# Kernel optimization log

Hardware: AMD Instinct MI355X
Metric: run time of the kernel (lower is better)

The kernel has to match this reference:

```python
import jax, jax.numpy as jnp
import numpy as np

B, N, D = 4, 1024, 1024
H = 16
RS, RC = 32, 32
MLP = int(D * 4.0)
EPS = 1e-6


def _ln(x):
    # LayerNorm with no scale/bias (flax defaults: eps=1e-6)
    m = jnp.mean(x, axis=-1, keepdims=True)
    v = jnp.mean(jnp.square(x - m), axis=-1, keepdims=True)
    return (x - m) * jax.lax.rsqrt(v + EPS)


def _rms(x, scale):
    rms = jnp.sqrt(jnp.mean(jnp.square(x), axis=-1, keepdims=True) + EPS)
    return scale * x / rms


def _modulate(x, shift, scale):
    return x * (1 + scale[:, None]) + shift[:, None]


def setup_inputs() -> dict:
    key = jax.random.key(0)
    ks = jax.random.split(key, 20)
    s = 0.02
    return {
        'x': jax.random.normal(ks[0], (B, N, D), jnp.float32),
        'c': jax.random.normal(ks[1], (B, D), jnp.float32),
        'cls_token': jax.random.normal(ks[2], (B, D), jnp.float32),
        'Wc': jax.random.normal(ks[3], (D, 6 * D), jnp.float32) * s,
        'bc': jax.random.normal(ks[4], (6 * D,), jnp.float32) * s,
        'Wqkv': jax.random.normal(ks[5], (D, 3 * D), jnp.float32) * s,
        'bqkv': jnp.zeros((3 * D,), jnp.float32),
        'Wo': jax.random.normal(ks[6], (D, D), jnp.float32) * s,
        'bo': jnp.zeros((D,), jnp.float32),
        'A_s': jax.random.normal(ks[7], (D, RS), jnp.float32) * s,
        'B_s': jax.random.normal(ks[8], (RS, D), jnp.float32) * s,
        'rms_s_scale': jnp.ones((D,), jnp.float32),
        'C_r': jax.random.normal(ks[9], (D, RC), jnp.float32) * s,
        'D_r': jax.random.normal(ks[10], (RC, D), jnp.float32) * s,
        'rms_c_scale': jnp.ones((D,), jnp.float32),
        'W1': jax.random.normal(ks[11], (D, MLP), jnp.float32) * s,
        'b1': jnp.zeros((MLP,), jnp.float32),
        'W2': jax.random.normal(ks[12], (MLP, D), jnp.float32) * s,
        'b2': jnp.zeros((D,), jnp.float32),
    }


def reference(x, c, cls_token, Wc, bc, Wqkv, bqkv, Wo, bo, A_s, B_s,
              rms_s_scale, C_r, D_r, rms_c_scale, W1, b1, W2, b2):
    hd = D // H
    # AdaLN conditioning
    c_proj = jax.nn.silu(c) @ Wc + bc                    # (B, 6D)
    shift_a, scale_a, gate_a, shift_m, scale_m, gate_m = jnp.split(c_proj, 6, axis=-1)

    # Self-attention branch
    x_norm = _modulate(_ln(x), shift_a, scale_a)         # (B, N, D)
    qkv = x_norm @ Wqkv + bqkv                           # (B, N, 3D)
    q, k, v = jnp.split(qkv, 3, axis=-1)
    q = q.reshape(B, N, H, hd).transpose(0, 2, 1, 3)     # (B, H, N, hd)
    k = k.reshape(B, N, H, hd).transpose(0, 2, 1, 3)
    v = v.reshape(B, N, H, hd).transpose(0, 2, 1, 3)
    attn_w = jax.nn.softmax(jnp.einsum('bhqd,bhkd->bhqk', q, k) * hd ** (-0.5), axis=-1)
    attn_out = jnp.einsum('bhqk,bhkd->bhqd', attn_w, v)
    attn_out = attn_out.transpose(0, 2, 1, 3).reshape(B, N, D)
    attn_out = attn_out @ Wo + bo
    Y = x + gate_a[:, None] * attn_out

    # Self-gram low-rank branch (residual)
    gram_s = (x @ A_s) @ B_s                             # (B, N, D)
    X_prime = _rms(gram_s, rms_s_scale) + Y

    # Cross-gram branch via CLS token (no residual)
    u_c = cls_token[:, :, None] * C_r[None]              # (B, D, RC)
    v_c = jnp.einsum('bnd,bdr->bnr', X_prime, u_c)       # (B, N, RC)
    gram_c = v_c @ D_r                                   # (B, N, D)
    Z = _rms(gram_c, rms_c_scale)

    # MLP branch
    z_norm = _modulate(_ln(Z), shift_m, scale_m)
    h = jax.nn.gelu(z_norm @ W1 + b1) @ W2 + b2
    return Z + gate_m[:, None] * h
```

## Files before the change

kernel.cpp:

```cpp
#include <hip/hip_runtime.h>
#include <stdint.h>

typedef float  f32x4  __attribute__((ext_vector_type(4)));
typedef short  s16x8  __attribute__((ext_vector_type(8)));
typedef __bf16 bf16x4 __attribute__((ext_vector_type(4)));
typedef __bf16 bf16x8 __attribute__((ext_vector_type(8)));

#define D_    1024
#define SIXD  6144
#define QSCALE 0.18033688011112042f

#define BAR() asm volatile("s_barrier" ::: "memory")

__device__ __forceinline__ f32x4 mfma_b(const s16x8 &a, const s16x8 &b, const f32x4 &c) {
  return __builtin_amdgcn_mfma_f32_16x16x32_bf16(a, b, c, 0, 0, 0);
}

__device__ __forceinline__ void gload_lds16(const void* g, void* l) {
  __builtin_amdgcn_global_load_lds(
      (const __attribute__((address_space(1))) uint32_t*)g,
      (__attribute__((address_space(3))) uint32_t*)l, 16, 0, 0);
}

__global__ __launch_bounds__(256)
void prep(const float* __restrict__ c, const float* __restrict__ Wc,
          const float* __restrict__ bc, float* __restrict__ cproj,
          const float* __restrict__ Wqkv, const float* __restrict__ Wo,
          const float* __restrict__ W1, const float* __restrict__ W2,
          __bf16* __restrict__ Wqkvt, __bf16* __restrict__ Wot,
          __bf16* __restrict__ W1t, __bf16* __restrict__ W2t)
{
  __shared__ __align__(16) char smem[33280];
  int tid = threadIdx.x;
  if (blockIdx.x < 192) {
    float* sc = (float*)smem;
    float (*tp)[4][32] = (float(*)[4][32])(smem + 16384);
    for (int i = tid; i < 4096; i += 256) {
      float v = c[i];
      sc[i] = v / (1.f + __expf(-v));
    }
    __syncthreads();
    int colo = tid & 31, kseg = tid >> 5;
    int col = blockIdx.x * 32 + colo;
    float a0 = 0.f, a1 = 0.f, a2 = 0.f, a3 = 0.f;
    for (int k = kseg * 128; k < kseg * 128 + 128; k++) {
      float w = Wc[(size_t)k * SIXD + col];
      a0 += sc[k] * w; a1 += sc[1024 + k] * w;
      a2 += sc[2048 + k] * w; a3 += sc[3072 + k] * w;
    }
    tp[kseg][0][colo] = a0; tp[kseg][1][colo] = a1;
    tp[kseg][2][colo] = a2; tp[kseg][3][colo] = a3;
    __syncthreads();
    if (kseg == 0) {
#pragma unroll
      for (int b = 0; b < 4; b++) {
        float s = bc[col];
#pragma unroll
        for (int g = 0; g < 8; g++) s += tp[g][b][colo];
        cproj[b * SIXD + col] = s;
      }
    }
    return;
  }
  int bid = blockIdx.x - 192;
  const float* W; __bf16* Wt; int Kdim, Ndim, lb;
  if (bid < 192)      { W = Wqkv; Wt = Wqkvt; Kdim = 1024; Ndim = 3072; lb = bid; }
  else if (bid < 256) { W = Wo;   Wt = Wot;   Kdim = 1024; Ndim = 1024; lb = bid - 192; }
  else if (bid < 512) { W = W1;   Wt = W1t;   Kdim = 1024; Ndim = 4096; lb = bid - 256; }
  else                { W = W2;   Wt = W2t;   Kdim = 4096; Ndim = 1024; lb = bid - 512; }
  int ntn = Ndim >> 6;
  int ktg = lb / ntn, nt = lb % ntn;
  __bf16* tt = (__bf16*)smem;
  const float* src = W + (size_t)(ktg * 256) * Ndim + nt * 64;
  int krow = tid >> 4, c4 = tid & 15;
#pragma unroll
  for (int t = 0; t < 4; t++) {
#pragma unroll
    for (int i = 0; i < 4; i++) {
      int k = i * 16 + krow;
      float4 v = ((const float4*)(src + (size_t)(t * 64 + k) * Ndim))[c4];
      __bf16* row = tt + (t * 64 + k) * 65 + c4 * 4;
      row[0] = (__bf16)v.x; row[1] = (__bf16)v.y;
      row[2] = (__bf16)v.z; row[3] = (__bf16)v.w;
    }
  }
  __syncthreads();
  __bf16* dst = Wt + (size_t)(nt * 64) * Kdim + ktg * 256;
  int n = tid >> 2, ks = (tid & 3) * 16;
#pragma unroll
  for (int t = 0; t < 4; t++) {
    bf16x8 lo, hi;
#pragma unroll
    for (int j = 0; j < 8; j++) {
      lo[j] = tt[(t * 64 + ks + j) * 65 + n];
      hi[j] = tt[(t * 64 + ks + 8 + j) * 65 + n];
    }
    __bf16* dp = dst + (size_t)n * Kdim + t * 64 + ks;
    *(bf16x8*)(dp) = lo;
    *(bf16x8*)(dp + 8) = hi;
  }
}

__global__ __launch_bounds__(256)
void ln_mod(const float* __restrict__ X, const float* __restrict__ cproj,
            int shift_off, int scale_off, __bf16* __restrict__ Out)
{
  int row = blockIdx.x;
  int b = row >> 10;
  int tid = threadIdx.x;
  const float4* xr = (const float4*)(X + (size_t)row * D_);
  float4 v = xr[tid];
  float s  = v.x + v.y + v.z + v.w;
  float s2 = v.x * v.x + v.y * v.y + v.z * v.z + v.w * v.w;
#pragma unroll
  for (int off = 1; off < 64; off <<= 1) {
    s  += __shfl_xor(s,  off, 64);
    s2 += __shfl_xor(s2, off, 64);
  }
  __shared__ float red[8];
  int wave = tid >> 6, lane = tid & 63;
  if (lane == 0) { red[wave] = s; red[4 + wave] = s2; }
  __syncthreads();
  s  = red[0] + red[1] + red[2] + red[3];
  s2 = red[4] + red[5] + red[6] + red[7];
  float mean = s * (1.f / D_);
  float var  = s2 * (1.f / D_) - mean * mean;
  float rstd = rsqrtf(var + 1e-6f);
  const float4* sh = (const float4*)(cproj + b * SIXD + shift_off);
  const float4* sc = (const float4*)(cproj + b * SIXD + scale_off);
  float4 shv = sh[tid], scv = sc[tid];
  bf16x4 o;
  o[0] = (__bf16)((v.x - mean) * rstd * (1.f + scv.x) + shv.x);
  o[1] = (__bf16)((v.y - mean) * rstd * (1.f + scv.y) + shv.y);
  o[2] = (__bf16)((v.z - mean) * rstd * (1.f + scv.z) + shv.z);
  o[3] = (__bf16)((v.w - mean) * rstd * (1.f + scv.w) + shv.w);
  *(bf16x4*)(Out + (size_t)row * D_ + tid * 4) = o;
}

template<int EPI, int NBUF>
__global__ __launch_bounds__(256)
void gemm_bt(const __bf16* __restrict__ A, const __bf16* __restrict__ Bt,
             const float* __restrict__ bias, const float* __restrict__ cproj,
             int gate_off, const float* __restrict__ resid,
             void* __restrict__ Cout, void* __restrict__ Cout2,
             void* __restrict__ Cout3, void* __restrict__ Cout4,
             int M, int N, int K, int SK)
{
  __shared__ __align__(16) __bf16 As[NBUF * 128 * 32];
  __shared__ __align__(16) __bf16 Bs[NBUF * 128 * 32];
  const int PD = NBUF - 1;
  int tilesN = N >> 7, tilesM = M >> 7;
  int npersk = tilesM * tilesN;
  int sk = blockIdx.x / npersk;
  int rest = blockIdx.x % npersk;
  int cpx = npersk >> 3;
  rest = (rest & 7) * cpx + (rest >> 3);
  int bm = rest / tilesN, bn = rest % tilesN;
  int Klen = K / SK, Kstart = sk * Klen;

  int tid = threadIdx.x;
  int lane = tid & 63, wave = tid >> 6;
  int lr = lane & 15, lg = lane >> 4;
  int wm = (wave >> 1) << 6, wn = (wave & 1) << 6;

  f32x4 acc[4][4] = {};

  int sr = tid >> 2, skb = tid & 3;
  int scol = ((skb ^ ((sr >> 1) & 3)) * 8);
  const __bf16* pa = A + (size_t)((bm << 7) + sr) * K + Kstart + scol;
  const __bf16* pb = Bt + (size_t)((bn << 7) + sr) * K + Kstart + scol;
  const size_t rstep = (size_t)64 * K;
  __bf16* la = As + tid * 8;
  __bf16* lb = Bs + tid * 8;

  auto STAGE = [&](int buf, int k0) {
    int bo = buf * 4096;
    gload_lds16(pa + k0, la + bo);
    gload_lds16(pa + rstep + k0, la + bo + 2048);
    gload_lds16(pb + k0, lb + bo);
    gload_lds16(pb + rstep + k0, lb + bo + 2048);
  };

  int nt = Klen >> 5;
#pragma unroll
  for (int p = 0; p < PD; p++) STAGE(p, p * 32);

  for (int t = 0; t < nt; t++) {
    if (t + PD < nt) STAGE((t + PD) % NBUF, (t + PD) * 32);
    int ahead = nt - 1 - t; if (ahead > PD) ahead = PD;
    if (ahead >= 3)      asm volatile("s_waitcnt vmcnt(12)" ::: "memory");
    else if (ahead == 2) asm volatile("s_waitcnt vmcnt(8)" ::: "memory");
    else if (ahead == 1) asm volatile("s_waitcnt vmcnt(4)" ::: "memory");
    else                 asm volatile("s_waitcnt vmcnt(0)" ::: "memory");
    BAR();
    const __bf16* Ac = As + (t % NBUF) * 4096;
    const __bf16* Bc = Bs + (t % NBUF) * 4096;
    s16x8 af[4], bfv[4];
#pragma unroll
    for (int m = 0; m < 4; m++) {
      int row = wm + m * 16 + lr;
      af[m] = *(const s16x8*)(Ac + row * 32 + ((lg ^ ((row >> 1) & 3)) * 8));
    }
#pragma unroll
    for (int n = 0; n < 4; n++) {
      int row = wn + n * 16 + lr;
      bfv[n] = *(const s16x8*)(Bc + row * 32 + ((lg ^ ((row >> 1) & 3)) * 8));
    }
    asm volatile("s_waitcnt lgkmcnt(0)" ::: "memory");
    __builtin_amdgcn_sched_barrier(0);
    BAR();
    __builtin_amdgcn_s_setprio(1);
#pragma unroll
    for (int m = 0; m < 4; m++)
#pragma unroll
      for (int n = 0; n < 4; n++)
        acc[m][n] = mfma_b(af[m], bfv[n], acc[m][n]);
    __builtin_amdgcn_s_setprio(0);
  }
  asm volatile("s_waitcnt vmcnt(0)" ::: "memory");

  int row0 = (bm << 7) + wm;
  int col0 = (bn << 7) + wn;
#pragma unroll
  for (int m = 0; m < 4; m++) {
#pragma unroll
    for (int n = 0; n < 4; n++) {
      int cc = col0 + n * 16 + lr;
      float bv = bias[cc];
#pragma unroll
      for (int r = 0; r < 4; r++) {
        int row = row0 + m * 16 + (lg << 2) + r;
        float v = acc[m][n][r] + bv;
        size_t idx = (size_t)row * N + cc;
        if (EPI == 0) {
          ((__bf16*)Cout)[idx] = (__bf16)v;
        } else if (EPI == 1) {
          int b = row >> 10;
          float g = cproj[b * SIXD + gate_off + cc];
          ((float*)Cout)[idx] = resid[idx] + g * v;
        }
      }
    }
  }
}

template<int EPI, int NT, int KD>
__global__ __launch_bounds__(512, 2)
void gemm256(const __bf16* __restrict__ A, const __bf16* __restrict__ Bt,
             const float* __restrict__ bias, const float* __restrict__ gcproj,
             void* __restrict__ Cout, void* __restrict__ Cout2,
             int M, int N)
{
  __shared__ __align__(16) __bf16 As[2 * 16384];
  __shared__ __align__(16) __bf16 Bs[2 * 16384];
  int tilesN = N >> 8, tilesM = M >> 8;
  int npersk = tilesM * tilesN;
  int sk = blockIdx.x / npersk;
  int rest = blockIdx.x % npersk;
  int cpx = npersk >> 3;
  rest = (rest & 7) * cpx + (rest >> 3);
  int bm = rest / tilesN, bn = rest % tilesN;
  int Kstart = sk * (NT * 64);

  int tid = threadIdx.x;
  int lane = tid & 63, wave = tid >> 6;
  int lr = lane & 15, lg = lane >> 4;
  int wr = wave >> 2, wc = wave & 3;

  f32x4 acc[8][4] = {};

  int srow = tid >> 3;
  int schunk = (tid & 7) ^ (srow & 7);
  const __bf16* pa = A  + (size_t)((bm << 8) + srow) * KD + Kstart + schunk * 8;
  const __bf16* pb = Bt + (size_t)((bn << 8) + srow) * KD + Kstart + schunk * 8;
  __bf16* la = As + tid * 8;
  __bf16* lb = Bs + tid * 8;

  auto SAq = [&](int t, int q) {
    gload_lds16(pa + (size_t)(q * 64) * KD + t * 64,
                la + (t & 1) * 16384 + q * 4096);
  };
  auto SBq = [&](int t, int q) {
    gload_lds16(pb + (size_t)(q * 64) * KD + t * 64,
                lb + (t & 1) * 16384 + q * 4096);
  };

#pragma unroll
  for (int q = 0; q < 4; q++) { SAq(0, q); }
#pragma unroll
  for (int q = 0; q < 4; q++) { SBq(0, q); }
#pragma unroll
  for (int q = 0; q < 4; q++) { SAq(1, q); }
#pragma unroll
  for (int q = 0; q < 4; q++) { SBq(1, q); }
  asm volatile("s_waitcnt vmcnt(8)" ::: "memory");
  BAR();

  int cc0 = ((lg ^ (lr & 7)) << 4);
  int cc1 = cc0 ^ 64;
  const char* aA = (const char*)As + (wr * 128 + lr) * 128;
  const char* aB = (const char*)Bs + (wc * 64 + lr) * 128;

  s16x8 alo[4][2], ahi[4][2], b0v[2][2], b1v[2][2];
#pragma unroll
  for (int m = 0; m < 4; m++) {
    alo[m][0] = *(const s16x8*)(aA + m * 2048 + cc0);
    alo[m][1] = *(const s16x8*)(aA + m * 2048 + cc1);
  }
#pragma unroll
  for (int n = 0; n < 2; n++) {
    b0v[n][0] = *(const s16x8*)(aB + n * 2048 + cc0);
    b0v[n][1] = *(const s16x8*)(aB + n * 2048 + cc1);
  }

  for (int t = 0; t < NT; t++) {
    const char* Ab = aA + (t & 1) * 32768;
    const char* Bb = aB + (t & 1) * 32768;

#pragma unroll
    for (int n = 0; n < 2; n++) {
      b1v[n][0] = *(const s16x8*)(Bb + 4096 + n * 2048 + cc0);
      b1v[n][1] = *(const s16x8*)(Bb + 4096 + n * 2048 + cc1);
    }
    __builtin_amdgcn_sched_barrier(0);
    __builtin_amdgcn_s_setprio(1);
#pragma unroll
    for (int m = 0; m < 4; m++)
#pragma unroll
      for (int n = 0; n < 2; n++) {
        acc[m][n] = mfma_b(alo[m][0], b0v[n][0], acc[m][n]);
        acc[m][n] = mfma_b(alo[m][1], b0v[n][1], acc[m][n]);
      }
    __builtin_amdgcn_s_setprio(0);
    asm volatile("s_waitcnt lgkmcnt(0)" ::: "memory");
    BAR();

#pragma unroll
    for (int m = 0; m < 4; m++) {
      ahi[m][0] = *(const s16x8*)(Ab + 8192 + m * 2048 + cc0);
      ahi[m][1] = *(const s16x8*)(Ab + 8192 + m * 2048 + cc1);
    }
    if (t + 2 < NT) { SBq(t + 2, 0); SBq(t + 2, 1); }
    __builtin_amdgcn_sched_barrier(0);
    __builtin_amdgcn_s_setprio(1);
#pragma unroll
    for (int m = 0; m < 4; m++)
#pragma unroll
      for (int n = 0; n < 2; n++) {
        acc[m][2 + n] = mfma_b(alo[m][0], b1v[n][0], acc[m][2 + n]);
        acc[m][2 + n] = mfma_b(alo[m][1], b1v[n][1], acc[m][2 + n]);
      }
    __builtin_amdgcn_s_setprio(0);
    asm volatile("s_waitcnt lgkmcnt(0)" ::: "memory");
    BAR();

    if (t + 2 < NT) {
      SBq(t + 2, 2); SBq(t + 2, 3);
      SAq(t + 2, 0); SAq(t + 2, 1); SAq(t + 2, 2); SAq(t + 2, 3);
    }
    __builtin_amdgcn_sched_barrier(0);
    __builtin_amdgcn_s_setprio(1);
#pragma unroll
    for (int m = 0; m < 4; m++)
#pragma unroll
      for (int n = 0; n < 2; n++) {
        acc[4 + m][2 + n] = mfma_b(ahi[m][0], b1v[n][0], acc[4 + m][2 + n]);
        acc[4 + m][2 + n] = mfma_b(ahi[m][1], b1v[n][1], acc[4 + m][2 + n]);
      }
#pragma unroll
    for (int m = 0; m < 4; m++)
#pragma unroll
      for (int n = 0; n < 2; n++) {
        acc[4 + m][n] = mfma_b(ahi[m][0], b0v[n][0], acc[4 + m][n]);
        acc[4 + m][n] = mfma_b(ahi[m][1], b0v[n][1], acc[4 + m][n]);
      }
    __builtin_amdgcn_s_setprio(0);
    if (t + 1 < NT) {
      if (t + 2 < NT) asm volatile("s_waitcnt vmcnt(8)" ::: "memory");
      else            asm volatile("s_waitcnt vmcnt(0)" ::: "memory");
      BAR();
      const char* An = aA + ((t + 1) & 1) * 32768;
      const char* Bn = aB + ((t + 1) & 1) * 32768;
#pragma unroll
      for (int m = 0; m < 4; m++) {
        alo[m][0] = *(const s16x8*)(An + m * 2048 + cc0);
        alo[m][1] = *(const s16x8*)(An + m * 2048 + cc1);
      }
#pragma unroll
      for (int n = 0; n < 2; n++) {
        b0v[n][0] = *(const s16x8*)(Bn + n * 2048 + cc0);
        b0v[n][1] = *(const s16x8*)(Bn + n * 2048 + cc1);
      }
    }
  }
  asm volatile("s_waitcnt lgkmcnt(0)" ::: "memory");

  int row0 = (bm << 8) + wr * 128;
  int col0 = (bn << 8) + wc * 64;
#pragma unroll
  for (int m = 0; m < 8; m++) {
#pragma unroll
    for (int n = 0; n < 4; n++) {
      int cc = col0 + n * 16 + lr;
      float bv;
      if (EPI == 6)      bv = (sk == 0) ? bias[cc] : 0.f;
      else               bv = bias[cc];
      if (EPI == 5 && cc >= 2048) {
        int rbase = row0 + m * 16 + (lg << 2);
        int dd = cc - 2048;
        int bb = rbase >> 10, ntok = rbase & 1023;
        bf16x4 o;
#pragma unroll
        for (int r = 0; r < 4; r++) o[r] = (__bf16)(acc[m][n][r] + bv);
        *(bf16x4*)((__bf16*)Cout2 + ((size_t)(bb << 10) + dd) * 1024 + ntok) = o;
        continue;
      }
#pragma unroll
      for (int r = 0; r < 4; r++) {
        int row = row0 + m * 16 + (lg << 2) + r;
        float v = acc[m][n][r] + bv;
        size_t idx = (size_t)row * N + cc;
        if (EPI == 2) {
          float u = 0.7978845608028654f * (v + 0.044715f * v * v * v);
          u = fminf(fmaxf(u, -15.f), 15.f);
          float e = __expf(2.f * u);
          float th = (e - 1.f) / (e + 1.f);
          ((__bf16*)Cout)[idx] = (__bf16)(0.5f * v * (1.f + th));
        } else if (EPI == 5) {
          float scq = (cc < 1024) ? QSCALE : 1.f;
          ((__bf16*)Cout)[idx] = (__bf16)(v * scq);
        } else if (EPI == 6) {
          int bb = row >> 10;
          float g = gcproj[bb * SIXD + 5120 + cc];
          atomicAdd((float*)Cout + idx, g * v);
        }
      }
    }
  }
}

__global__ __launch_bounds__(512, 4)
void attn_flash(const __bf16* __restrict__ qkv, const __bf16* __restrict__ Vt,
                __bf16* __restrict__ O)
{
  __shared__ __align__(16) __bf16 Kl[2][64 * 64];
  __shared__ __align__(16) __bf16 Vl[2][64 * 64];
  __shared__ __align__(16) __bf16 Pl[8][16 * 64];

  int bid = ((blockIdx.x & 7) << 6) | (blockIdx.x >> 3);
  int qt = bid & 7, h = (bid >> 3) & 15, b = bid >> 7;
  int tid = threadIdx.x, wave = tid >> 6, lane = tid & 63;
  int lr = lane & 15, lg = lane >> 4;

  size_t tok0 = (size_t)b * 1024;
  int qrow = qt * 128 + wave * 16 + lr;
  const __bf16* qptr = qkv + (tok0 + qrow) * 3072 + h * 64;
  s16x8 qf0 = *(const s16x8*)(qptr + lg * 8);
  s16x8 qf1 = *(const s16x8*)(qptr + 32 + lg * 8);

  float l_acc[4] = {0.f, 0.f, 0.f, 0.f};
  f32x4 oacc[4] = {};

  const __bf16* kbase = qkv + tok0 * 3072 + 1024 + h * 64;
  const __bf16* vbase = Vt + ((size_t)(b * 16 + h) * 64) * 1024;

  int skey = tid >> 3, sdb = tid & 7;
  const __bf16* ksrc = kbase + (size_t)skey * 3072 + ((sdb ^ (skey & 7)) * 8);
  const __bf16* vsrc = vbase + (size_t)skey * 1024 + ((sdb ^ (skey & 7)) * 8);
  __bf16* klp = &Kl[0][0] + tid * 8;
  __bf16* vlp = &Vl[0][0] + tid * 8;
  __bf16* pl = &Pl[wave][0];

  auto STAGE = [&](int buf, int kk) {
    gload_lds16(ksrc + (size_t)kk * 3072, klp + buf * 4096);
    gload_lds16(vsrc + kk, vlp + buf * 4096);
  };

  STAGE(0, 0);
  int cur = 0;
  for (int k0 = 0; k0 < 1024; k0 += 64) {
    int kn = (k0 + 64 < 1024) ? (k0 + 64) : k0;
    STAGE(cur ^ 1, kn);
    asm volatile("s_waitcnt vmcnt(2)" ::: "memory");
    BAR();
    const __bf16* K_ = &Kl[cur][0];
    const __bf16* V_ = &Vl[cur][0];

    f32x4 s[4];
    __builtin_amdgcn_s_setprio(1);
#pragma unroll
    for (int n = 0; n < 4; n++) {
      int key = n * 16 + lr;
      int kx = key & 7;
      s16x8 kf0 = *(const s16x8*)(K_ + key * 64 + ((lg ^ kx) * 8));
      s16x8 kf1 = *(const s16x8*)(K_ + key * 64 + (((4 + lg) ^ kx) * 8));
      f32x4 sa = {0.f, 0.f, 0.f, 0.f};
      sa = mfma_b(qf0, kf0, sa);
      sa = mfma_b(qf1, kf1, sa);
      s[n] = sa;
    }
    __builtin_amdgcn_s_setprio(0);

#pragma unroll
    for (int n = 0; n < 4; n++)
#pragma unroll
      for (int r = 0; r < 4; r++)
        s[n][r] = exp2f(s[n][r]);
#pragma unroll
    for (int r = 0; r < 4; r++)
      l_acc[r] += (s[0][r] + s[1][r]) + (s[2][r] + s[3][r]);

#pragma unroll
    for (int n = 0; n < 4; n++)
#pragma unroll
      for (int r = 0; r < 4; r++) {
        int prow = lg * 4 + r;
        int key = n * 16 + lr;
        int idx = prow * 64 + (((key >> 3) ^ (prow & 7)) * 8) + (key & 7);
        pl[idx] = (__bf16)s[n][r];
      }
    asm volatile("s_waitcnt lgkmcnt(0)" ::: "memory");
    __builtin_amdgcn_sched_barrier(0);
    s16x8 pf0 = *(const s16x8*)(pl + lr * 64 + ((lg ^ (lr & 7)) * 8));
    s16x8 pf1 = *(const s16x8*)(pl + lr * 64 + (((4 + lg) ^ (lr & 7)) * 8));

    __builtin_amdgcn_s_setprio(1);
#pragma unroll
    for (int dt = 0; dt < 4; dt++) {
      int vrow = dt * 16 + lr, rx = vrow & 7;
      s16x8 vf0 = *(const s16x8*)(V_ + vrow * 64 + ((lg ^ rx) * 8));
      s16x8 vf1 = *(const s16x8*)(V_ + vrow * 64 + (((4 + lg) ^ rx) * 8));
      oacc[dt] = mfma_b(pf0, vf0, oacc[dt]);
      oacc[dt] = mfma_b(pf1, vf1, oacc[dt]);
    }
    __builtin_amdgcn_s_setprio(0);
    asm volatile("s_waitcnt lgkmcnt(0)" ::: "memory");
    __builtin_amdgcn_sched_barrier(0);
    BAR();
    cur ^= 1;
  }
  asm volatile("s_waitcnt vmcnt(0)" ::: "memory");

  float rinv[4];
#pragma unroll
  for (int r = 0; r < 4; r++) {
    float v = l_acc[r];
#pragma unroll
    for (int off = 1; off < 16; off <<= 1) v += __shfl_xor(v, off, 64);
    rinv[r] = 1.f / v;
  }

  int orow = qt * 128 + wave * 16 + (lg << 2);
#pragma unroll
  for (int dt = 0; dt < 4; dt++)
#pragma unroll
    for (int r = 0; r < 4; r++) {
      float v = oacc[dt][r] * rinv[r];
      O[(tok0 + orow + r) * 1024 + h * 64 + dt * 16 + lr] = (__bf16)v;
    }
}

__global__ __launch_bounds__(256)
void gram_fused(const float* __restrict__ X, const float* __restrict__ Y,
                const float* __restrict__ cls,
                const float* __restrict__ A_s, const float* __restrict__ B_s,
                const float* __restrict__ rms_s,
                const float* __restrict__ C_r, const float* __restrict__ D_r,
                const float* __restrict__ rms_c,
                const float* __restrict__ cproj,
                float* __restrict__ Z, __bf16* __restrict__ Znorm)
{
  __shared__ float xs[4][D_];
  __shared__ float tp[8][4][32];
  __shared__ float t1[4][32];
  __shared__ float red[4][4];
  __shared__ float red2[4][4][2];
  int row0 = blockIdx.x * 4;
  int b = row0 >> 10;
  int tid = threadIdx.x;
  int wv = tid >> 6;

  f32x4 cv = *(const f32x4*)(cls + (size_t)b * D_ + tid * 4);
  f32x4 yv[4];
#pragma unroll
  for (int rr = 0; rr < 4; rr++) {
    ((f32x4*)xs[rr])[tid] = *(const f32x4*)(X + (size_t)(row0 + rr) * D_ + tid * 4);
    yv[rr] = *(const f32x4*)(Y + (size_t)(row0 + rr) * D_ + tid * 4);
  }
  __syncthreads();

  {
    int r = tid & 31, seg = tid >> 5;
    float a0 = 0.f, a1 = 0.f, a2 = 0.f, a3 = 0.f;
    const float* ap = A_s + r;
    for (int d = seg * 128; d < seg * 128 + 128; d++) {
      float w = ap[d * 32];
      a0 += xs[0][d] * w; a1 += xs[1][d] * w;
      a2 += xs[2][d] * w; a3 += xs[3][d] * w;
    }
    tp[seg][0][r] = a0; tp[seg][1][r] = a1; tp[seg][2][r] = a2; tp[seg][3][r] = a3;
  }
  __syncthreads();
  if (tid < 128) {
    int rr = tid >> 5, r = tid & 31;
    float sv = 0.f;
#pragma unroll
    for (int g = 0; g < 8; g++) sv += tp[g][rr][r];
    t1[rr][r] = sv;
  }
  __syncthreads();

  f32x4 g[4] = {};
  for (int r = 0; r < 32; r++) {
    f32x4 bv = *(const f32x4*)(B_s + (size_t)r * D_ + tid * 4);
    g[0] += t1[0][r] * bv; g[1] += t1[1][r] * bv;
    g[2] += t1[2][r] * bv; g[3] += t1[3][r] * bv;
  }
  float ssl[4];
#pragma unroll
  for (int rr = 0; rr < 4; rr++)
    ssl[rr] = g[rr][0]*g[rr][0] + g[rr][1]*g[rr][1] + g[rr][2]*g[rr][2] + g[rr][3]*g[rr][3];
#pragma unroll
  for (int off = 1; off < 64; off <<= 1)
#pragma unroll
    for (int rr = 0; rr < 4; rr++) ssl[rr] += __shfl_xor(ssl[rr], off, 64);
  if ((tid & 63) == 0) {
#pragma unroll
    for (int rr = 0; rr < 4; rr++) red[wv][rr] = ssl[rr];
  }
  __syncthreads();
  {
    f32x4 scv = *(const f32x4*)(rms_s + tid * 4);
#pragma unroll
    for (int rr = 0; rr < 4; rr++) {
      float ss = red[0][rr] + red[1][rr] + red[2][rr] + red[3][rr];
      float rs = rsqrtf(ss * (1.f / D_) + 1e-6f);
      f32x4 xp = scv * g[rr] * rs + yv[rr];
      ((f32x4*)xs[rr])[tid] = xp * cv;
    }
  }
  __syncthreads();

  {
    int r = tid & 31, seg = tid >> 5;
    float a0 = 0.f, a1 = 0.f, a2 = 0.f, a3 = 0.f;
    const float* cp = C_r + r;
    for (int d = seg * 128; d < seg * 128 + 128; d++) {
      float w = cp[d * 32];
      a0 += xs[0][d] * w; a1 += xs[1][d] * w;
      a2 += xs[2][d] * w; a3 += xs[3][d] * w;
    }
    tp[seg][0][r] = a0; tp[seg][1][r] = a1; tp[seg][2][r] = a2; tp[seg][3][r] = a3;
  }
  __syncthreads();
  if (tid < 128) {
    int rr = tid >> 5, r = tid & 31;
    float sv = 0.f;
#pragma unroll
    for (int g2i = 0; g2i < 8; g2i++) sv += tp[g2i][rr][r];
    t1[rr][r] = sv;
  }
  __syncthreads();

  f32x4 g2[4] = {};
  for (int r = 0; r < 32; r++) {
    f32x4 bv = *(const f32x4*)(D_r + (size_t)r * D_ + tid * 4);
    g2[0] += t1[0][r] * bv; g2[1] += t1[1][r] * bv;
    g2[2] += t1[2][r] * bv; g2[3] += t1[3][r] * bv;
  }
#pragma unroll
  for (int rr = 0; rr < 4; rr++)
    ssl[rr] = g2[rr][0]*g2[rr][0] + g2[rr][1]*g2[rr][1] + g2[rr][2]*g2[rr][2] + g2[rr][3]*g2[rr][3];
#pragma unroll
  for (int off = 1; off < 64; off <<= 1)
#pragma unroll
    for (int rr = 0; rr < 4; rr++) ssl[rr] += __shfl_xor(ssl[rr], off, 64);
  if ((tid & 63) == 0) {
#pragma unroll
    for (int rr = 0; rr < 4; rr++) red[wv][rr] = ssl[rr];
  }
  __syncthreads();
  f32x4 z[4];
  {
    f32x4 scv = *(const f32x4*)(rms_c + tid * 4);
#pragma unroll
    for (int rr = 0; rr < 4; rr++) {
      float ss = red[0][rr] + red[1][rr] + red[2][rr] + red[3][rr];
      float rs = rsqrtf(ss * (1.f / D_) + 1e-6f);
      z[rr] = scv * g2[rr] * rs;
    }
  }

  float s1l[4], s2l[4];
#pragma unroll
  for (int rr = 0; rr < 4; rr++) {
    s1l[rr] = z[rr][0] + z[rr][1] + z[rr][2] + z[rr][3];
    s2l[rr] = z[rr][0]*z[rr][0] + z[rr][1]*z[rr][1] + z[rr][2]*z[rr][2] + z[rr][3]*z[rr][3];
  }
#pragma unroll
  for (int off = 1; off < 64; off <<= 1)
#pragma unroll
    for (int rr = 0; rr < 4; rr++) {
      s1l[rr] += __shfl_xor(s1l[rr], off, 64);
      s2l[rr] += __shfl_xor(s2l[rr], off, 64);
    }
  if ((tid & 63) == 0) {
#pragma unroll
    for (int rr = 0; rr < 4; rr++) { red2[wv][rr][0] = s1l[rr]; red2[wv][rr][1] = s2l[rr]; }
  }
  __syncthreads();
  f32x4 shv = *(const f32x4*)(cproj + b * SIXD + 3072 + tid * 4);
  f32x4 scm = *(const f32x4*)(cproj + b * SIXD + 4096 + tid * 4);
#pragma unroll
  for (int rr = 0; rr < 4; rr++) {
    float S  = red2[0][rr][0] + red2[1][rr][0] + red2[2][rr][0] + red2[3][rr][0];
    float S2 = red2[0][rr][1] + red2[1][rr][1] + red2[2][rr][1] + red2[3][rr][1];
    float mean = S * (1.f / D_);
    float var  = S2 * (1.f / D_) - mean * mean;
    float rstd = rsqrtf(var + 1e-6f);
    f32x4 zn = (z[rr] - mean) * rstd * (scm + 1.f) + shv;
    *(f32x4*)(Z + (size_t)(row0 + rr) * D_ + tid * 4) = z[rr];
    bf16x4 o;
#pragma unroll
    for (int i = 0; i < 4; i++) o[i] = (__bf16)zn[i];
    *(bf16x4*)(Znorm + (size_t)(row0 + rr) * D_ + tid * 4) = o;
  }
}

extern "C" void kernel_launch(void* const* d_in, const int* in_sizes, int n_in,
                              void* d_out, int out_size, void* d_ws, size_t ws_size,
                              hipStream_t stream)
{
  const float* x     = (const float*)d_in[0];
  const float* c     = (const float*)d_in[1];
  const float* cls   = (const float*)d_in[2];
  const float* Wc    = (const float*)d_in[3];
  const float* bc    = (const float*)d_in[4];
  const float* Wqkv  = (const float*)d_in[5];
  const float* bqkv  = (const float*)d_in[6];
  const float* Wo    = (const float*)d_in[7];
  const float* bo    = (const float*)d_in[8];
  const float* A_s   = (const float*)d_in[9];
  const float* B_s   = (const float*)d_in[10];
  const float* rms_s = (const float*)d_in[11];
  const float* C_r   = (const float*)d_in[12];
  const float* D_r   = (const float*)d_in[13];
  const float* rms_c = (const float*)d_in[14];
  const float* W1    = (const float*)d_in[15];
  const float* b1    = (const float*)d_in[16];
  const float* W2    = (const float*)d_in[17];
  const float* b2    = (const float*)d_in[18];
  float* out = (float*)d_out;

  float* ws = (float*)d_ws;
  __bf16* Wqkvt = (__bf16*)(ws + 0);
  __bf16* Wot   = (__bf16*)(ws + 1572864);
  __bf16* W1t   = (__bf16*)(ws + 2097152);
  __bf16* W2t   = (__bf16*)(ws + 4194304);
  float*  cproj = ws + 6291456;
  __bf16* xnorm = (__bf16*)(ws + 6316032);
  __bf16* qkv   = (__bf16*)(ws + 8413184);
  __bf16* Vt    = (__bf16*)(ws + 14704640);
  __bf16* h1    = (__bf16*)(ws + 8413184);
  __bf16* attno = (__bf16*)(ws + 16801792);
  float*  Ybuf  = ws + 18898944;

  prep<<<960, 256, 0, stream>>>(c, Wc, bc, cproj,
                                Wqkv, Wo, W1, W2, Wqkvt, Wot, W1t, W2t);
  ln_mod<<<4096, 256, 0, stream>>>(x, cproj, 0, 1024, xnorm);
  gemm256<5, 16, 1024><<<192, 512, 0, stream>>>(xnorm, Wqkvt, bqkv, nullptr,
                                                qkv, Vt, 4096, 3072);
  attn_flash<<<512, 512, 0, stream>>>(qkv, Vt, attno);
  gemm_bt<1, 4><<<256, 256, 0, stream>>>(attno, Wot, bo, cproj, 2048, x,
                                         Ybuf, nullptr, nullptr, nullptr,
                                         4096, 1024, 1024, 1);
  gram_fused<<<1024, 256, 0, stream>>>(x, Ybuf, cls, A_s, B_s, rms_s,
                                       C_r, D_r, rms_c, cproj, out, xnorm);
  gemm256<2, 16, 1024><<<256, 512, 0, stream>>>(xnorm, W1t, b1, nullptr,
                                                h1, nullptr, 4096, 4096);
  gemm256<6, 16, 4096><<<256, 512, 0, stream>>>(h1, W2t, b2, cproj,
                                                out, nullptr, 4096, 1024);
}
```

Before: 284.2 us.

## Move QKV and W2 GEMMs to 128-tile kernel, drop split-K atomics

The QKV projection moves from the 256-tile gemm256 kernel (192 blocks) to the 128-tile gemm_bt kernel with 3-stage buffering (768 blocks), carrying its Q-scaling and V-transpose epilogue along. The W2 down-projection stops using a split-K gemm256 variant with atomicAdd into the output. It now uses gemm_bt with the gated residual epilogue, writing out in place once over the full K=4096. The aim is better CU occupancy for the QKV GEMM and no atomic read-modify-write traffic on the output. The cost is lower per-block data reuse from smaller tiles, and only 256 blocks for the long-K W2 GEMM.

After: 284.6 us. No clear change (+0.1%).

```diff
diff --git a/kernel.cpp b/kernel.cpp
--- a/kernel.cpp
+++ b/kernel.cpp
@@ -143,20 +143,17 @@
              const float* __restrict__ bias, const float* __restrict__ cproj,
              int gate_off, const float* __restrict__ resid,
              void* __restrict__ Cout, void* __restrict__ Cout2,
-             void* __restrict__ Cout3, void* __restrict__ Cout4,
-             int M, int N, int K, int SK)
+             int M, int N, int K)
 {
   __shared__ __align__(16) __bf16 As[NBUF * 128 * 32];
   __shared__ __align__(16) __bf16 Bs[NBUF * 128 * 32];
   const int PD = NBUF - 1;
   int tilesN = N >> 7, tilesM = M >> 7;
   int npersk = tilesM * tilesN;
-  int sk = blockIdx.x / npersk;
   int rest = blockIdx.x % npersk;
   int cpx = npersk >> 3;
   rest = (rest & 7) * cpx + (rest >> 3);
   int bm = rest / tilesN, bn = rest % tilesN;
-  int Klen = K / SK, Kstart = sk * Klen;
 
   int tid = threadIdx.x;
   int lane = tid & 63, wave = tid >> 6;
@@ -167,8 +164,8 @@
 
   int sr = tid >> 2, skb = tid & 3;
   int scol = ((skb ^ ((sr >> 1) & 3)) * 8);
-  const __bf16* pa = A + (size_t)((bm << 7) + sr) * K + Kstart + scol;
-  const __bf16* pb = Bt + (size_t)((bn << 7) + sr) * K + Kstart + scol;
+  const __bf16* pa = A + (size_t)((bm << 7) + sr) * K + scol;
+  const __bf16* pb = Bt + (size_t)((bn << 7) + sr) * K + scol;
   const size_t rstep = (size_t)64 * K;
   __bf16* la = As + tid * 8;
   __bf16* lb = Bs + tid * 8;
@@ -181,7 +178,7 @@
     gload_lds16(pb + rstep + k0, lb + bo + 2048);
   };
 
-  int nt = Klen >> 5;
+  int nt = K >> 5;
 #pragma unroll
   for (int p = 0; p < PD; p++) STAGE(p, p * 32);
 
@@ -227,6 +224,16 @@
     for (int n = 0; n < 4; n++) {
       int cc = col0 + n * 16 + lr;
       float bv = bias[cc];
+      if (EPI == 5 && cc >= 2048) {
+        int rbase = row0 + m * 16 + (lg << 2);
+        int dd = cc - 2048;
+        int bb = rbase >> 10, ntok = rbase & 1023;
+        bf16x4 o;
+#pragma unroll
+        for (int r = 0; r < 4; r++) o[r] = (__bf16)(acc[m][n][r] + bv);
+        *(bf16x4*)((__bf16*)Cout2 + ((size_t)(bb << 10) + dd) * 1024 + ntok) = o;
+        continue;
+      }
 #pragma unroll
       for (int r = 0; r < 4; r++) {
         int row = row0 + m * 16 + (lg << 2) + r;
@@ -238,6 +245,9 @@
           int b = row >> 10;
           float g = cproj[b * SIXD + gate_off + cc];
           ((float*)Cout)[idx] = resid[idx] + g * v;
+        } else if (EPI == 5) {
+          float scq = (cc < 1024) ? QSCALE : 1.f;
+          ((__bf16*)Cout)[idx] = (__bf16)(v * scq);
         }
       }
     }
@@ -247,20 +257,17 @@
 template<int EPI, int NT, int KD>
 __global__ __launch_bounds__(512, 2)
 void gemm256(const __bf16* __restrict__ A, const __bf16* __restrict__ Bt,
-             const float* __restrict__ bias, const float* __restrict__ gcproj,
-             void* __restrict__ Cout, void* __restrict__ Cout2,
-             int M, int N)
+             const float* __restrict__ bias,
+             void* __restrict__ Cout, int M, int N)
 {
   __shared__ __align__(16) __bf16 As[2 * 16384];
   __shared__ __align__(16) __bf16 Bs[2 * 16384];
   int tilesN = N >> 8, tilesM = M >> 8;
   int npersk = tilesM * tilesN;
-  int sk = blockIdx.x / npersk;
   int rest = blockIdx.x % npersk;
   int cpx = npersk >> 3;
   rest = (rest & 7) * cpx + (rest >> 3);
   int bm = rest / tilesN, bn = rest % tilesN;
-  int Kstart = sk * (NT * 64);
 
   int tid = threadIdx.x;
   int lane = tid & 63, wave = tid >> 6;
@@ -271,8 +278,8 @@
 
   int srow = tid >> 3;
   int schunk = (tid & 7) ^ (srow & 7);
-  const __bf16* pa = A  + (size_t)((bm << 8) + srow) * KD + Kstart + schunk * 8;
-  const __bf16* pb = Bt + (size_t)((bn << 8) + srow) * KD + Kstart + schunk * 8;
+  const __bf16* pa = A  + (size_t)((bm << 8) + srow) * KD + schunk * 8;
+  const __bf16* pb = Bt + (size_t)((bn << 8) + srow) * KD + schunk * 8;
   __bf16* la = As + tid * 8;
   __bf16* lb = Bs + tid * 8;
 
@@ -402,19 +409,7 @@
 #pragma unroll
     for (int n = 0; n < 4; n++) {
       int cc = col0 + n * 16 + lr;
-      float bv;
-      if (EPI == 6)      bv = (sk == 0) ? bias[cc] : 0.f;
-      else               bv = bias[cc];
-      if (EPI == 5 && cc >= 2048) {
-        int rbase = row0 + m * 16 + (lg << 2);
-        int dd = cc - 2048;
-        int bb = rbase >> 10, ntok = rbase & 1023;
-        bf16x4 o;
-#pragma unroll
-        for (int r = 0; r < 4; r++) o[r] = (__bf16)(acc[m][n][r] + bv);
-        *(bf16x4*)((__bf16*)Cout2 + ((size_t)(bb << 10) + dd) * 1024 + ntok) = o;
-        continue;
-      }
+      float bv = bias[cc];
 #pragma unroll
       for (int r = 0; r < 4; r++) {
         int row = row0 + m * 16 + (lg << 2) + r;
@@ -426,13 +421,8 @@
           float e = __expf(2.f * u);
           float th = (e - 1.f) / (e + 1.f);
           ((__bf16*)Cout)[idx] = (__bf16)(0.5f * v * (1.f + th));
-        } else if (EPI == 5) {
-          float scq = (cc < 1024) ? QSCALE : 1.f;
-          ((__bf16*)Cout)[idx] = (__bf16)(v * scq);
-        } else if (EPI == 6) {
-          int bb = row >> 10;
-          float g = gcproj[bb * SIXD + 5120 + cc];
-          atomicAdd((float*)Cout + idx, g * v);
+        } else {
+          ((__bf16*)Cout)[idx] = (__bf16)v;
         }
       }
     }
@@ -768,16 +758,14 @@
   prep<<<960, 256, 0, stream>>>(c, Wc, bc, cproj,
                                 Wqkv, Wo, W1, W2, Wqkvt, Wot, W1t, W2t);
   ln_mod<<<4096, 256, 0, stream>>>(x, cproj, 0, 1024, xnorm);
-  gemm256<5, 16, 1024><<<192, 512, 0, stream>>>(xnorm, Wqkvt, bqkv, nullptr,
-                                                qkv, Vt, 4096, 3072);
+  gemm_bt<5, 3><<<768, 256, 0, stream>>>(xnorm, Wqkvt, bqkv, nullptr, 0, nullptr,
+                                         qkv, Vt, 4096, 3072, 1024);
   attn_flash<<<512, 512, 0, stream>>>(qkv, Vt, attno);
   gemm_bt<1, 4><<<256, 256, 0, stream>>>(attno, Wot, bo, cproj, 2048, x,
-                                         Ybuf, nullptr, nullptr, nullptr,
-                                         4096, 1024, 1024, 1);
+                                         Ybuf, nullptr, 4096, 1024, 1024);
   gram_fused<<<1024, 256, 0, stream>>>(x, Ybuf, cls, A_s, B_s, rms_s,
                                        C_r, D_r, rms_c, cproj, out, xnorm);
-  gemm256<2, 16, 1024><<<256, 512, 0, stream>>>(xnorm, W1t, b1, nullptr,
-                                                h1, nullptr, 4096, 4096);
-  gemm256<6, 16, 4096><<<256, 512, 0, stream>>>(h1, W2t, b2, cproj,
-                                                out, nullptr, 4096, 1024);
-}
+  gemm256<2, 16, 1024><<<256, 512, 0, stream>>>(xnorm, W1t, b1, h1, 4096, 4096);
+  gemm_bt<1, 4><<<256, 256, 0, stream>>>(h1, W2t, b2, cproj, 5120, out,
+                                         out, nullptr, 4096, 1024, 4096);
+}
```
